# Kernel tuning notes

Hardware: AMD Instinct MI355X
Metric: run time of the kernel (lower is better)

Reference implementation:

```python
import jax, jax.numpy as jnp
import numpy as np

NUM_HEADS = 16
HEAD_DIM = 64
SCALE = 1.0 / np.sqrt(HEAD_DIM).astype(np.float32)


def _clinear(xr, xi, wr, wi):
    # complex matmul: (xr + i xi) @ (wr + i wi)
    yr = jnp.dot(xr, wr) - jnp.dot(xi, wi)
    yi = jnp.dot(xr, wi) + jnp.dot(xi, wr)
    return yr, yi


def setup_inputs() -> dict:
    key = jax.random.key(0)
    ks = jax.random.split(key, 12)
    B, L, S, C = 2, 2048, 2048, 1024
    glorot = 1.0 / np.sqrt(C)
    inp = {
        'inputs_real': jax.random.normal(ks[0], (B, L, C), jnp.float32),
        'inputs_imag': jax.random.normal(ks[1], (B, L, C), jnp.float32),
        'context_real': jax.random.normal(ks[2], (B, S, C), jnp.float32),
        'context_imag': jax.random.normal(ks[3], (B, S, C), jnp.float32),
        'wq_r': jax.random.normal(ks[4], (C, C), jnp.float32) * glorot,
        'wq_i': jax.random.normal(ks[5], (C, C), jnp.float32) * glorot,
        'wk_r': jax.random.normal(ks[6], (C, C), jnp.float32) * glorot,
        'wk_i': jax.random.normal(ks[7], (C, C), jnp.float32) * glorot,
        'wv_r': jax.random.normal(ks[8], (C, C), jnp.float32) * glorot,
        'wv_i': jax.random.normal(ks[9], (C, C), jnp.float32) * glorot,
        'wo_r': jax.random.normal(ks[10], (C, C), jnp.float32) * glorot,
        'wo_i': jax.random.normal(ks[11], (C, C), jnp.float32) * glorot,
        'bo_r': jnp.zeros((C,), jnp.float32),
        'bo_i': jnp.zeros((C,), jnp.float32),
    }
    return inp


def reference(inputs_real, inputs_imag, context_real, context_imag,
              wq_r, wq_i, wk_r, wk_i, wv_r, wv_i, wo_r, wo_i, bo_r, bo_i):
    B, L, C = inputs_real.shape
    S = context_real.shape[1]
    H, D = NUM_HEADS, HEAD_DIM

    qr, qi = _clinear(inputs_real, inputs_imag, wq_r, wq_i)
    kr, ki = _clinear(context_real, context_imag, wk_r, wk_i)
    vr, vi = _clinear(context_real, context_imag, wv_r, wv_i)

    qr = qr.reshape(B, L, H, D); qi = qi.reshape(B, L, H, D)
    kr = kr.reshape(B, S, H, D); ki = ki.reshape(B, S, H, D)
    vr = vr.reshape(B, S, H, D); vi = vi.reshape(B, S, H, D)

    # real part of q . conj-free inner product: qr.kr + qi.ki, scaled
    scores = (jnp.einsum('blhd,bshd->bhls', qr, kr)
              + jnp.einsum('blhd,bshd->bhls', qi, ki)) * SCALE
    attn = jax.nn.softmax(scores, axis=-1)

    out_r = jnp.einsum('bhls,bshd->blhd', attn, vr).reshape(B, L, C)
    out_i = jnp.einsum('bhls,bshd->blhd', attn, vi).reshape(B, L, C)

    yr, yi = _clinear(out_r, out_i, wo_r, wo_i)
    yr = yr + bo_r
    yi = yi + bo_i
    # stack real/imag parts: shape [2, B, L, C]
    return jnp.stack([yr, yi], axis=0)
```

## Files before the change

### kernel.cpp

```cpp
#include <hip/hip_runtime.h>

#define BB 2
#define LQ 2048
#define SK 2048
#define CH 1024
#define NH 16
#define HD 64
#define GK 2048
#define MM 4096
#define ATT_SCALE 0.125f

typedef _Float16 f16x8 __attribute__((ext_vector_type(8)));
typedef float f32x4 __attribute__((ext_vector_type(4)));
typedef unsigned short u16x8 __attribute__((ext_vector_type(8)));

__device__ __forceinline__ unsigned short h2u(_Float16 h) {
    union { _Float16 h; unsigned short u; } v; v.h = h; return v.u;
}
__device__ __forceinline__ void gload16(const _Float16* g, unsigned short* l) {
    __builtin_amdgcn_global_load_lds(
        (const __attribute__((address_space(1))) void*)g,
        (__attribute__((address_space(3))) void*)l, 16, 0, 0);
}

__device__ __forceinline__ float dpp_max16(float x) {
    union { float f; int i; } v, r;
    v.f = x;
    r.i = __builtin_amdgcn_update_dpp(v.i, v.i, 0xB1, 0xF, 0xF, false);
    v.f = fmaxf(v.f, r.f);
    r.i = __builtin_amdgcn_update_dpp(v.i, v.i, 0x4E, 0xF, 0xF, false);
    v.f = fmaxf(v.f, r.f);
    r.i = __builtin_amdgcn_update_dpp(v.i, v.i, 0x141, 0xF, 0xF, false);
    v.f = fmaxf(v.f, r.f);
    r.i = __builtin_amdgcn_update_dpp(v.i, v.i, 0x140, 0xF, 0xF, false);
    v.f = fmaxf(v.f, r.f);
    return v.f;
}

__device__ __forceinline__ int swzi(int row, int colh, int ldh) {
    return row * ldh + (colh ^ ((row & 7) << 3));
}

struct PackXEnt { const float* r; const float* i; _Float16* dst; };
struct PackXBatch { PackXEnt e[2]; };

__global__ __launch_bounds__(256) void pack_x_kernel(PackXBatch b)
{
    PackXEnt e = b.e[blockIdx.z];
    const size_t total = (size_t)MM * GK;
    for (size_t idx = (size_t)blockIdx.x * 256 + threadIdx.x; idx < total;
         idx += (size_t)gridDim.x * 256) {
        size_t m = idx >> 11;
        int c = (int)(idx & 2047);
        float v = (c < CH) ? e.r[m * CH + c] : e.i[m * CH + (c - CH)];
        e.dst[idx] = (_Float16)v;
    }
}

struct PackWEnt { const float* a; const float* b; float signb; _Float16* dst; };
struct PackWBatch { PackWEnt e[8]; };

__global__ __launch_bounds__(256) void pack_w_kernel(PackWBatch bt)
{
    PackWEnt e = bt.e[blockIdx.z];
    const int k0 = blockIdx.x * 32;
    const int n0 = blockIdx.y * 32;
    const float* src = (k0 < CH) ? e.a : e.b;
    const float sign = (k0 < CH) ? 1.f : e.signb;
    const int kk = k0 & (CH - 1);

    __shared__ float sT[32][33];
    const int t = threadIdx.x;
    const int tx = t & 31, ty = t >> 5;

    #pragma unroll
    for (int r = 0; r < 4; r++) {
        int kl = ty + r * 8;
        sT[kl][tx] = src[(size_t)(kk + kl) * CH + n0 + tx] * sign;
    }
    __syncthreads();
    #pragma unroll
    for (int r = 0; r < 4; r++) {
        int nl = ty + r * 8;
        e.dst[(size_t)(n0 + nl) * GK + k0 + tx] = (_Float16)sT[tx][nl];
    }
}

struct GemmEnt { const _Float16* A; const _Float16* Bt; void* out;
                 const float* bias; int mode; int part; };
struct GemmBatch { GemmEnt e[6]; };

#define NT   (GK / 32)
#define BUFH 12288

#define SWZ(x) ((x) ^ ((((x) >> 7) & 3) << 4))

__global__ __launch_bounds__(512, 2) void mfma_cgemm(GemmBatch bt)
{
    GemmEnt e = bt.e[blockIdx.z];
    __shared__ unsigned short lds[4 * BUFH];

    const int t    = threadIdx.x;
    const int wave = t >> 6;
    const int lane = t & 63;
    const int lm   = lane & 15;
    const int quad = lane >> 4;
    const int wr   = wave >> 1;
    const int wc   = wave & 1;

    const int m0 = blockIdx.y * 256;
    const int n0 = blockIdx.x * 128;

    int srow[2], scol[2];
    #pragma unroll
    for (int L = 0; L < 2; L++) {
        int p = (L * 512 + t) * 16;
        int q = SWZ(p);
        srow[L] = q >> 6;
        scol[L] = (q >> 1) & 31;
    }

    const _Float16* gA = e.A  + (size_t)m0 * GK;
    const _Float16* gB = e.Bt + (size_t)n0 * GK;

    auto stage = [&](int kt) {
        unsigned short* base = lds + (kt & 3) * BUFH;
        #pragma unroll
        for (int L = 0; L < 2; L++)
            gload16(gA + (size_t)srow[L] * GK + kt * 32 + scol[L],
                    base + (L * 512 + t) * 8);
        gload16(gB + (size_t)srow[0] * GK + kt * 32 + scol[0],
                base + 8192 + t * 8);
    };

    const int qA    = (wr * 64 + lm) * 64 + quad * 16;
    const int physA = SWZ(qA) >> 1;
    const int qB    = (wc * 64 + lm) * 64 + quad * 16;
    const int physB = (SWZ(qB) >> 1) + 8192;

    f32x4 acc[4][4] = {};

    stage(0); stage(1); stage(2);
    asm volatile("s_waitcnt vmcnt(6)" ::: "memory");
    __builtin_amdgcn_s_barrier();

    for (int kt = 0; kt < NT; ++kt) {
        const unsigned short* buf = lds + (kt & 3) * BUFH;
        f16x8 af[4], bf[4];
        #pragma unroll
        for (int i = 0; i < 4; i++)
            af[i] = *(const f16x8*)&buf[physA + i * 512];
        #pragma unroll
        for (int j = 0; j < 4; j++)
            bf[j] = *(const f16x8*)&buf[physB + j * 512];

        if (kt + 3 < NT) stage(kt + 3);

        __builtin_amdgcn_s_barrier();
        asm volatile("s_waitcnt lgkmcnt(0)" ::: "memory");
        __builtin_amdgcn_s_setprio(1);
        #pragma unroll
        for (int i = 0; i < 4; i++)
            #pragma unroll
            for (int j = 0; j < 4; j++)
                acc[i][j] = __builtin_amdgcn_mfma_f32_16x16x32_f16(
                    af[i], bf[j], acc[i][j], 0, 0, 0);
        __builtin_amdgcn_s_setprio(0);

        if (kt < NT - 3)       asm volatile("s_waitcnt vmcnt(6)" ::: "memory");
        else if (kt == NT - 3) asm volatile("s_waitcnt vmcnt(3)" ::: "memory");
        else if (kt == NT - 2) asm volatile("s_waitcnt vmcnt(0)" ::: "memory");
        __builtin_amdgcn_s_barrier();
    }

    const int mode = e.mode, part = e.part;
    #pragma unroll
    for (int j = 0; j < 4; j++) {
        int gcol = n0 + wc * 64 + j * 16 + lm;
        float bv = (mode == 2 && e.bias) ? e.bias[gcol] : 0.f;
        #pragma unroll
        for (int i = 0; i < 4; i++) {
            int growb = m0 + wr * 64 + i * 16 + quad * 4;
            #pragma unroll
            for (int reg = 0; reg < 4; reg++) {
                int grow = growb + reg;
                float v = acc[i][j][reg];
                if (mode == 2) {
                    ((float*)e.out)[(size_t)grow * CH + gcol] = v + bv;
                } else {
                    int b = grow >> 11, l = grow & 2047;
                    int h = gcol >> 6, dd = gcol & 63;
                    size_t off;
                    if (mode == 0)
                        off = (((size_t)(b * NH + h)) * LQ + l) * 128 + part * 64 + dd;
                    else
                        off = (((size_t)(b * NH + h)) * 128 + part * 64 + dd) * SK + l;
                    ((_Float16*)e.out)[off] = (_Float16)v;
                }
            }
        }
    }
}

__global__ __launch_bounds__(512, 2) void attn_mfma(
    const _Float16* __restrict__ Qp, const _Float16* __restrict__ Kp,
    const _Float16* __restrict__ Vt, _Float16* __restrict__ Aattn)
{
    __shared__ unsigned short lds[33792];
    unsigned short* sP = lds;
    unsigned short* sK = lds + 16384;
    unsigned short* sV = lds + 24576;

    const int t    = threadIdx.x;
    const int w    = t >> 6;
    const int lane = t & 63;
    const int lm   = lane & 15;
    const int quad = lane >> 4;

    const int bx  = blockIdx.x;
    const int bid = (bx & 7) * 32 + (bx >> 3);
    const int mt  = bid & 7;
    const int h   = (bid >> 3) & 15;
    const int b   = bid >> 7;

    const _Float16* qb = Qp + (((size_t)(b * NH + h)) * LQ + (size_t)mt * 256) * 128;
    const _Float16* kb = Kp + ((size_t)(b * NH + h)) * SK * 128;
    const _Float16* vb = Vt + ((size_t)(b * NH + h)) * 128 * SK;

    for (int idx = t; idx < 16 * 64; idx += 512) {
        int row = 128 + (idx >> 6);
        int col = idx & 63;
        sV[row * 64 + (col ^ ((row & 7) << 3))] = 0x3C00;
    }

    f16x8 qf[2][4];
    #pragma unroll
    for (int i = 0; i < 2; i++)
        #pragma unroll
        for (int kk = 0; kk < 4; kk++)
            qf[i][kk] = *(const f16x8*)(qb + (size_t)(w * 32 + i * 16 + lm) * 128
                                           + kk * 32 + quad * 8);

    u16x8 kreg[2], vreg[2];
    #pragma unroll
    for (int p = 0; p < 2; p++) {
        int idx = p * 512 + t;
        int r = idx >> 4, sg = idx & 15;
        kreg[p] = *(const u16x8*)(kb + (size_t)r * 128 + sg * 8);
        int rv = idx >> 3, sv = idx & 7;
        vreg[p] = *(const u16x8*)(vb + (size_t)rv * SK + sv * 8);
    }

    f32x4 oacc[2][9] = {};
    float m_st[2][4];
    #pragma unroll
    for (int i = 0; i < 2; i++)
        #pragma unroll
        for (int r = 0; r < 4; r++) m_st[i][r] = -1e30f;

    const float SC2 = ATT_SCALE * 1.44269504f;

    for (int it = 0; it < SK / 64; ++it) {
        __syncthreads();
        #pragma unroll
        for (int p = 0; p < 2; p++) {
            int idx = p * 512 + t;
            int r = idx >> 4, sg = idx & 15;
            *(u16x8*)&sK[swzi(r, sg * 8, 128)] = kreg[p];
            int rv = idx >> 3, sv = idx & 7;
            *(u16x8*)&sV[swzi(rv, sv * 8, 64)] = vreg[p];
        }
        __syncthreads();

        if (it + 1 < SK / 64) {
            int s0n = (it + 1) * 64;
            #pragma unroll
            for (int p = 0; p < 2; p++) {
                int idx = p * 512 + t;
                int r = idx >> 4, sg = idx & 15;
                kreg[p] = *(const u16x8*)(kb + (size_t)(s0n + r) * 128 + sg * 8);
                int rv = idx >> 3, sv = idx & 7;
                vreg[p] = *(const u16x8*)(vb + (size_t)rv * SK + s0n + sv * 8);
            }
        }

        f32x4 sacc[2][4] = {};
        #pragma unroll
        for (int kk = 0; kk < 4; kk++) {
            f16x8 bfr[4];
            #pragma unroll
            for (int j = 0; j < 4; j++)
                bfr[j] = *(const f16x8*)&sK[swzi(j * 16 + lm, kk * 32 + quad * 8, 128)];
            #pragma unroll
            for (int i = 0; i < 2; i++)
                #pragma unroll
                for (int j = 0; j < 4; j++)
                    sacc[i][j] = __builtin_amdgcn_mfma_f32_16x16x32_f16(
                        qf[i][kk], bfr[j], sacc[i][j], 0, 0, 0);
        }

        float mx[2][4];
        #pragma unroll
        for (int i = 0; i < 2; i++)
            #pragma unroll
            for (int r = 0; r < 4; r++) {
                float m4 = fmaxf(fmaxf(sacc[i][0][r], sacc[i][1][r]),
                                 fmaxf(sacc[i][2][r], sacc[i][3][r]));
                mx[i][r] = dpp_max16(m4) * SC2;
            }
        int need = 0;
        #pragma unroll
        for (int i = 0; i < 2; i++)
            #pragma unroll
            for (int r = 0; r < 4; r++)
                need |= (mx[i][r] > m_st[i][r] + 8.0f) ? 1 : 0;
        if (__any(need)) {
            #pragma unroll
            for (int i = 0; i < 2; i++)
                #pragma unroll
                for (int r = 0; r < 4; r++) {
                    float mnew = fmaxf(m_st[i][r], mx[i][r]);
                    float al = exp2f(m_st[i][r] - mnew);
                    m_st[i][r] = mnew;
                    #pragma unroll
                    for (int j2 = 0; j2 < 9; j2++)
                        oacc[i][j2][r] *= al;
                }
        }
        #pragma unroll
        for (int i = 0; i < 2; i++)
            #pragma unroll
            for (int r = 0; r < 4; r++) {
                float mcur = m_st[i][r];
                int rowp = w * 32 + i * 16 + quad * 4 + r;
                #pragma unroll
                for (int j = 0; j < 4; j++) {
                    float p = exp2f(sacc[i][j][r] * SC2 - mcur);
                    sP[swzi(rowp, j * 16 + lm, 64)] = h2u((_Float16)p);
                }
            }

        #pragma unroll
        for (int kk = 0; kk < 2; kk++) {
            f16x8 pf[2], vf[9];
            #pragma unroll
            for (int i = 0; i < 2; i++)
                pf[i] = *(const f16x8*)&sP[swzi(w * 32 + i * 16 + lm, kk * 32 + quad * 8, 64)];
            #pragma unroll
            for (int j2 = 0; j2 < 9; j2++)
                vf[j2] = *(const f16x8*)&sV[swzi(j2 * 16 + lm, kk * 32 + quad * 8, 64)];
            #pragma unroll
            for (int i = 0; i < 2; i++)
                #pragma unroll
                for (int j2 = 0; j2 < 9; j2++)
                    oacc[i][j2] = __builtin_amdgcn_mfma_f32_16x16x32_f16(
                        pf[i], vf[j2], oacc[i][j2], 0, 0, 0);
        }
    }

    #pragma unroll
    for (int i = 0; i < 2; i++) {
        #pragma unroll
        for (int r = 0; r < 4; r++) {
            float inv = 1.f / oacc[i][8][r];
            int ml = w * 32 + i * 16 + quad * 4 + r;
            size_t row = (size_t)b * LQ + (size_t)mt * 256 + ml;
            #pragma unroll
            for (int j2 = 0; j2 < 8; j2++) {
                int d = j2 * 16 + lm;
                int dcol = (d < HD) ? h * HD + d : CH + h * HD + (d - HD);
                Aattn[row * GK + dcol] = (_Float16)(oacc[i][j2][r] * inv);
            }
        }
    }
}

extern "C" void kernel_launch(void* const* d_in, const int* in_sizes, int n_in,
                              void* d_out, int out_size, void* d_ws, size_t ws_size,
                              hipStream_t stream)
{
    const float* in_r = (const float*)d_in[0];
    const float* in_i = (const float*)d_in[1];
    const float* cx_r = (const float*)d_in[2];
    const float* cx_i = (const float*)d_in[3];
    const float* wq_r = (const float*)d_in[4];
    const float* wq_i = (const float*)d_in[5];
    const float* wk_r = (const float*)d_in[6];
    const float* wk_i = (const float*)d_in[7];
    const float* wv_r = (const float*)d_in[8];
    const float* wv_i = (const float*)d_in[9];
    const float* wo_r = (const float*)d_in[10];
    const float* wo_i = (const float*)d_in[11];
    const float* bo_r = (const float*)d_in[12];
    const float* bo_i = (const float*)d_in[13];

    _Float16* ws = (_Float16*)d_ws;
    const size_t A_ELEMS = (size_t)MM * GK;
    const size_t B_ELEMS = (size_t)CH * GK;
    const size_t H_ELEMS = (size_t)BB * NH * LQ * 128;

    _Float16* Ain   = ws;
    _Float16* Aattn = ws;
    _Float16* Actx  = Ain + A_ELEMS;
    _Float16* Bp    = Actx + A_ELEMS;
    _Float16* Qp    = Bp + 8 * B_ELEMS;
    _Float16* Kp    = Qp + H_ELEMS;
    _Float16* Vt    = Kp + H_ELEMS;

    _Float16* Bq_r = Bp + 0 * B_ELEMS;
    _Float16* Bq_i = Bp + 1 * B_ELEMS;
    _Float16* Bk_r = Bp + 2 * B_ELEMS;
    _Float16* Bk_i = Bp + 3 * B_ELEMS;
    _Float16* Bv_r = Bp + 4 * B_ELEMS;
    _Float16* Bv_i = Bp + 5 * B_ELEMS;
    _Float16* Bo_r = Bp + 6 * B_ELEMS;
    _Float16* Bo_i = Bp + 7 * B_ELEMS;

    float* out = (float*)d_out;
    float* yr = out;
    float* yi = out + (size_t)MM * CH;

    PackXBatch px;
    px.e[0] = { in_r, in_i, Ain  };
    px.e[1] = { cx_r, cx_i, Actx };
    pack_x_kernel<<<dim3(4096, 1, 2), 256, 0, stream>>>(px);

    PackWBatch pw;
    pw.e[0] = { wq_r, wq_i, -1.f, Bq_r };
    pw.e[1] = { wq_i, wq_r,  1.f, Bq_i };
    pw.e[2] = { wk_r, wk_i, -1.f, Bk_r };
    pw.e[3] = { wk_i, wk_r,  1.f, Bk_i };
    pw.e[4] = { wv_r, wv_i, -1.f, Bv_r };
    pw.e[5] = { wv_i, wv_r,  1.f, Bv_i };
    pw.e[6] = { wo_r, wo_i, -1.f, Bo_r };
    pw.e[7] = { wo_i, wo_r,  1.f, Bo_i };
    pack_w_kernel<<<dim3(GK / 32, CH / 32, 8), 256, 0, stream>>>(pw);

    GemmBatch gq;
    gq.e[0] = { Ain,  Bq_r, Qp, nullptr, 0, 0 };
    gq.e[1] = { Ain,  Bq_i, Qp, nullptr, 0, 1 };
    gq.e[2] = { Actx, Bk_r, Kp, nullptr, 0, 0 };
    gq.e[3] = { Actx, Bk_i, Kp, nullptr, 0, 1 };
    gq.e[4] = { Actx, Bv_r, Vt, nullptr, 1, 0 };
    gq.e[5] = { Actx, Bv_i, Vt, nullptr, 1, 1 };
    mfma_cgemm<<<dim3(CH / 128, MM / 256, 6), 512, 0, stream>>>(gq);

    attn_mfma<<<dim3(BB * NH * (LQ / 256)), 512, 0, stream>>>(Qp, Kp, Vt, Aattn);

    GemmBatch go;
    go.e[0] = { Aattn, Bo_r, yr, bo_r, 2, 0 };
    go.e[1] = { Aattn, Bo_i, yi, bo_i, 2, 1 };
    for (int z = 2; z < 6; z++) go.e[z] = go.e[0];
    mfma_cgemm<<<dim3(CH / 128, MM / 256, 2), 512, 0, stream>>>(go);
}
```

Baseline: 477.3 us.

## Load GEMM A fragments directly to registers and vectorize fp16 packing

```diff
diff --git a/kernel.cpp b/kernel.cpp
--- a/kernel.cpp
+++ b/kernel.cpp
@@ -47,13 +47,21 @@
 __global__ __launch_bounds__(256) void pack_x_kernel(PackXBatch b)
 {
     PackXEnt e = b.e[blockIdx.z];
-    const size_t total = (size_t)MM * GK;
-    for (size_t idx = (size_t)blockIdx.x * 256 + threadIdx.x; idx < total;
-         idx += (size_t)gridDim.x * 256) {
-        size_t m = idx >> 11;
-        int c = (int)(idx & 2047);
-        float v = (c < CH) ? e.r[m * CH + c] : e.i[m * CH + (c - CH)];
-        e.dst[idx] = (_Float16)v;
+    const size_t total8 = (size_t)MM * GK / 8;
+    for (size_t s = (size_t)blockIdx.x * 256 + threadIdx.x; s < total8;
+         s += (size_t)gridDim.x * 256) {
+        size_t m = s >> 8;
+        int c8 = (int)(s & 255) * 8;
+        const float* src = (c8 < CH) ? (e.r + m * CH + c8)
+                                     : (e.i + m * CH + (c8 - CH));
+        float4 a = *(const float4*)(src);
+        float4 c = *(const float4*)(src + 4);
+        u16x8 o;
+        o[0] = h2u((_Float16)a.x); o[1] = h2u((_Float16)a.y);
+        o[2] = h2u((_Float16)a.z); o[3] = h2u((_Float16)a.w);
+        o[4] = h2u((_Float16)c.x); o[5] = h2u((_Float16)c.y);
+        o[6] = h2u((_Float16)c.z); o[7] = h2u((_Float16)c.w);
+        *(u16x8*)(e.dst + s * 8) = o;
     }
 }
 
@@ -91,14 +99,12 @@
 struct GemmBatch { GemmEnt e[6]; };
 
 #define NT   (GK / 32)
-#define BUFH 12288
-
 #define SWZ(x) ((x) ^ ((((x) >> 7) & 3) << 4))
 
 __global__ __launch_bounds__(512, 2) void mfma_cgemm(GemmBatch bt)
 {
     GemmEnt e = bt.e[blockIdx.z];
-    __shared__ unsigned short lds[4 * BUFH];
+    __shared__ unsigned short lds[4 * 4096];
 
     const int t    = threadIdx.x;
     const int wave = t >> 6;
@@ -111,66 +117,62 @@
     const int m0 = blockIdx.y * 256;
     const int n0 = blockIdx.x * 128;
 
-    int srow[2], scol[2];
-    #pragma unroll
-    for (int L = 0; L < 2; L++) {
-        int p = (L * 512 + t) * 16;
-        int q = SWZ(p);
-        srow[L] = q >> 6;
-        scol[L] = (q >> 1) & 31;
-    }
-
-    const _Float16* gA = e.A  + (size_t)m0 * GK;
+    const int pq   = SWZ(t * 16);
+    const int sbrow = pq >> 6;
+    const int sbcol = (pq >> 1) & 31;
+
     const _Float16* gB = e.Bt + (size_t)n0 * GK;
 
-    auto stage = [&](int kt) {
-        unsigned short* base = lds + (kt & 3) * BUFH;
-        #pragma unroll
-        for (int L = 0; L < 2; L++)
-            gload16(gA + (size_t)srow[L] * GK + kt * 32 + scol[L],
-                    base + (L * 512 + t) * 8);
-        gload16(gB + (size_t)srow[0] * GK + kt * 32 + scol[0],
-                base + 8192 + t * 8);
+    const _Float16* gAr[4];
+    #pragma unroll
+    for (int i = 0; i < 4; i++)
+        gAr[i] = e.A + (size_t)(m0 + wr * 64 + i * 16 + lm) * GK + quad * 8;
+
+    const int physB = SWZ((wc * 64 + lm) * 64 + quad * 16) >> 1;
+
+    f32x4 acc[4][4] = {};
+    f16x8 afA[4], afB[4];
+
+    auto stageB = [&](int kt) {
+        gload16(gB + (size_t)sbrow * GK + kt * 32 + sbcol,
+                lds + (kt & 3) * 4096 + t * 8);
     };
 
-    const int qA    = (wr * 64 + lm) * 64 + quad * 16;
-    const int physA = SWZ(qA) >> 1;
-    const int qB    = (wc * 64 + lm) * 64 + quad * 16;
-    const int physB = (SWZ(qB) >> 1) + 8192;
-
-    f32x4 acc[4][4] = {};
-
-    stage(0); stage(1); stage(2);
-    asm volatile("s_waitcnt vmcnt(6)" ::: "memory");
+    #pragma unroll
+    for (int i = 0; i < 4; i++) afA[i] = *(const f16x8*)(gAr[i]);
+    stageB(0); stageB(1); stageB(2);
+    asm volatile("s_waitcnt vmcnt(2)" ::: "memory");
     __builtin_amdgcn_s_barrier();
 
-    for (int kt = 0; kt < NT; ++kt) {
-        const unsigned short* buf = lds + (kt & 3) * BUFH;
-        f16x8 af[4], bf[4];
-        #pragma unroll
-        for (int i = 0; i < 4; i++)
-            af[i] = *(const f16x8*)&buf[physA + i * 512];
+    auto kstep = [&](int kt, f16x8 (&use)[4], f16x8 (&pre)[4]) {
+        const unsigned short* buf = lds + (kt & 3) * 4096;
+        f16x8 bf[4];
         #pragma unroll
         for (int j = 0; j < 4; j++)
             bf[j] = *(const f16x8*)&buf[physB + j * 512];
-
-        if (kt + 3 < NT) stage(kt + 3);
-
-        __builtin_amdgcn_s_barrier();
-        asm volatile("s_waitcnt lgkmcnt(0)" ::: "memory");
+        if (kt + 1 < NT) {
+            #pragma unroll
+            for (int i = 0; i < 4; i++)
+                pre[i] = *(const f16x8*)(gAr[i] + (kt + 1) * 32);
+        }
+        if (kt + 3 < NT) stageB(kt + 3);
+        if (kt < NT - 3)       asm volatile("s_waitcnt vmcnt(5)" ::: "memory");
+        else if (kt <  NT - 1) asm volatile("s_waitcnt vmcnt(4)" ::: "memory");
+        else                   asm volatile("s_waitcnt vmcnt(0)" ::: "memory");
         __builtin_amdgcn_s_setprio(1);
         #pragma unroll
         for (int i = 0; i < 4; i++)
             #pragma unroll
             for (int j = 0; j < 4; j++)
                 acc[i][j] = __builtin_amdgcn_mfma_f32_16x16x32_f16(
-                    af[i], bf[j], acc[i][j], 0, 0, 0);
+                    use[i], bf[j], acc[i][j], 0, 0, 0);
         __builtin_amdgcn_s_setprio(0);
-
-        if (kt < NT - 3)       asm volatile("s_waitcnt vmcnt(6)" ::: "memory");
-        else if (kt == NT - 3) asm volatile("s_waitcnt vmcnt(3)" ::: "memory");
-        else if (kt == NT - 2) asm volatile("s_waitcnt vmcnt(0)" ::: "memory");
         __builtin_amdgcn_s_barrier();
+    };
+
+    for (int kt = 0; kt < NT; kt += 2) {
+        kstep(kt,     afA, afB);
+        kstep(kt + 1, afB, afA);
     }
 
     const int mode = e.mode, part = e.part;
```

After: 610.0 us. +27.8%, slower.
